# Kernel optimization log

Hardware: AMD Instinct MI355X
Metric: run time of the kernel (lower is better)

Reference implementation:

```python
import jax, jax.numpy as jnp
import numpy as np

B, T, L = 16, 64, 64
DIN, D, DC, A = 512, 512, 512, 256


def setup_inputs() -> dict:
    key = jax.random.key(0)
    ks = jax.random.split(key, 16)
    g = lambda k, shape, fan: jax.random.normal(k, shape, jnp.float32) / np.float32(np.sqrt(fan))
    return {
        "X": jax.random.normal(ks[0], (B, T, DIN), jnp.float32),
        "context": jax.random.normal(ks[1], (B, L, DC), jnp.float32),
        "parent_t_seq": jax.random.randint(ks[2], (B, T), 0, T),
        "context_mask": jnp.zeros((B, L), jnp.int32),
        "mask": jnp.ones((B, T), jnp.float32),
        # fused gate weights, gate order [i, f, c, o] along last axis
        "Wx": g(ks[3], (DIN, 4 * D), DIN),
        "bx": jnp.zeros((4 * D,), jnp.float32),
        "U": g(ks[4], (D, 4 * D), D),
        "C": g(ks[5], (DC, 4 * D), DC),
        "P": g(ks[6], (D, 4 * D), D),
        "H": g(ks[7], (D, 4 * D), D),
        # context attention
        "att_ctx_W1": g(ks[8], (DC, A), DC),
        "att_b1": jnp.zeros((A,), jnp.float32),
        "att_h_W1": g(ks[9], (D, A), D),
        "att_W2": g(ks[10], (A,), A),
        "att_b2": jnp.zeros((), jnp.float32),
        # history attention
        "hatt_hist_W": g(ks[11], (D, A), D),
        "hatt_hist_b": jnp.zeros((A,), jnp.float32),
        "hatt_h_W1": g(ks[12], (D, A), D),
        "hatt_W2": g(ks[13], (A,), A),
        "hatt_b2": jnp.zeros((), jnp.float32),
    }


def reference(X, context, parent_t_seq, context_mask, mask,
              Wx, bx, U, C, P, H,
              att_ctx_W1, att_b1, att_h_W1, att_W2, att_b2,
              hatt_hist_W, hatt_hist_b, hatt_h_W1, hatt_W2, hatt_b2):
    Bb, Tt, _ = X.shape
    Dd = U.shape[0]
    x4 = X @ Wx + bx                                 # [B,T,4D] precomputed input gates
    ctx_trans = context @ att_ctx_W1 + att_b1        # [B,L,A]
    ts = jnp.arange(Tt)
    batch_idx = jnp.arange(Bb)

    def step(carry, inp):
        h, c, hist = carry                           # h,c [B,D]; hist [B,T,D]
        t, xg, m, par = inp                          # xg [B,4D], m [B], par [B]
        # --- attention over encoder context ---
        ah = jnp.tanh(ctx_trans + (h @ att_h_W1)[:, None, :])   # [B,L,A]
        raw = ah @ att_W2 + att_b2                               # [B,L]
        raw = jnp.where(context_mask > 0, -jnp.inf, raw)
        catt = jax.nn.softmax(raw, axis=-1)
        ctx_vec = jnp.einsum('bl,blc->bc', catt, context)        # [B,DC]
        # --- attention over decoding history (positions < t) ---
        hh = jnp.tanh(hist @ hatt_hist_W + hatt_hist_b + (h @ hatt_h_W1)[:, None, :])  # [B,T,A]
        hraw = hh @ hatt_W2 + hatt_b2                            # [B,T]
        hmask = (ts < t).astype(X.dtype)                         # [T]
        hexp = jnp.exp(hraw - jnp.max(hraw, axis=-1, keepdims=True)) * hmask
        hw = hexp / (jnp.sum(hexp, axis=-1, keepdims=True) + 1e-7)
        h_ctx = jnp.where(t > 0, jnp.einsum('bt,btd->bd', hw, hist), 0.0)
        # --- parent hidden state feed ---
        par_h = jnp.where(t > 0, hist[batch_idx, par], 0.0)      # [B,D]
        # --- fused LSTM gates (tree attention path: U, C, P, H terms) ---
        g = xg + h @ U + ctx_vec @ C + par_h @ P + h_ctx @ H     # [B,4D]
        gi, gf, gc, go = jnp.split(g, 4, axis=-1)
        i = jax.nn.sigmoid(gi)
        f = jax.nn.sigmoid(gf)
        o = jax.nn.sigmoid(go)
        c_new = f * c + i * jnp.tanh(gc)
        h_new = o * jnp.tanh(c_new)
        mm = m[:, None]
        h_new = (1 - mm) * h + mm * h_new
        c_new = (1 - mm) * c + mm * c_new
        hist = jax.lax.dynamic_update_slice(hist, h_new[:, None, :], (0, t, 0))
        return (h_new, c_new, hist), (h_new, c_new, ctx_vec)

    h0 = jnp.zeros((Bb, Dd), X.dtype)
    c0 = jnp.zeros((Bb, Dd), X.dtype)
    hist0 = jnp.zeros((Bb, Tt, Dd), X.dtype)
    xs = (ts, jnp.swapaxes(x4, 0, 1), mask.T, parent_t_seq.T)
    _, (hs, cs, ctxs) = jax.lax.scan(step, (h0, c0, hist0), xs)
    # back to batch-major
    return (jnp.swapaxes(hs, 0, 1), jnp.swapaxes(cs, 0, 1), jnp.swapaxes(ctxs, 0, 1))
```

## Files before the change

### kernel.cpp

```cpp
#include <hip/hip_runtime.h>
#include <cmath>

#define NWG 256
#define NT  256

#define WS_FLAGS 0
#define WS_HC    8192
#define WS_CT    16384
#define WS_CACHE 278528
#define WS_HIST  540672

#define OUT_HS  0
#define OUT_CS  524288
#define OUT_CTX 1048576

#define LDS_WT   0
#define LDS_ZS   20544
#define LDS_SCR  28800
#define LDS_GLD  30848
#define LDS_ATT  30976
#define LDS_FLOATS 32448

typedef float vf4 __attribute__((ext_vector_type(4)));
typedef float vf2 __attribute__((ext_vector_type(2)));

struct CAParams {
  const float* X; const float* ctx; const int* parent; const int* cmask; const float* mask;
  const float* Wx; const float* bx; const float* U; const float* C; const float* P; const float* H;
  const float* acW1; const float* ab1; const float* ahW1; const float* aW2; const float* ab2;
  const float* hhW; const float* hhb; const float* hthW1; const float* hW2; const float* hb2;
  float* out; float* ws;
};

__device__ __forceinline__ float tanh_f(float x) {
  x = fminf(15.f, fmaxf(-15.f, x));
  float e = __expf(2.f * x);
  return (e - 1.f) / (e + 1.f);
}
__device__ __forceinline__ float sigm_f(float x) { return 1.f / (1.f + __expf(-x)); }
__device__ __forceinline__ float wsum(float v) {
  #pragma unroll
  for (int m = 32; m; m >>= 1) v += __shfl_xor(v, m, 64);
  return v;
}
__device__ __forceinline__ float wmax(float v) {
  #pragma unroll
  for (int m = 32; m; m >>= 1) v = fmaxf(v, __shfl_xor(v, m, 64));
  return v;
}
__device__ __forceinline__ float hsum32(float v) {
  #pragma unroll
  for (int m = 16; m; m >>= 1) v += __shfl_xor(v, m, 64);
  return v;
}

__device__ __forceinline__ void bst(float* a, float v) {
  asm volatile("global_store_dword %0, %1, off sc0 sc1" :: "v"(a), "v"(v) : "memory");
}
__device__ __forceinline__ void bst4(float* a, vf4 v) {
  asm volatile("global_store_dwordx4 %0, %1, off sc0 sc1" :: "v"(a), "v"(v) : "memory");
}
__device__ __forceinline__ void bld4x4(vf4* r, const float* p0, const float* p1,
                                       const float* p2, const float* p3) {
  asm volatile(
    "global_load_dwordx4 %0, %4, off sc0 sc1\n"
    "global_load_dwordx4 %1, %5, off sc0 sc1\n"
    "global_load_dwordx4 %2, %6, off sc0 sc1\n"
    "global_load_dwordx4 %3, %7, off sc0 sc1\n"
    "s_waitcnt vmcnt(0)"
    : "=&v"(r[0]), "=&v"(r[1]), "=&v"(r[2]), "=&v"(r[3])
    : "v"(p0), "v"(p1), "v"(p2), "v"(p3) : "memory");
}

__global__ void __launch_bounds__(NT, 1) condatt_kernel(CAParams p) {
  extern __shared__ float lds[];
  float* wt   = lds + LDS_WT;
  float* zs   = lds + LDS_ZS;
  float* scr  = lds + LDS_SCR;
  float* gld  = lds + LDS_GLD;
  float* aw   = lds + LDS_ATT;
  float* av2  = lds + LDS_ATT + 256;
  float* abv  = lds + LDS_ATT + 512;
  float* araw = lds + LDS_ATT + 768;
  float* asmx = lds + LDS_ATT + 832;
  float* arawZ= lds + LDS_ATT + 896;
  float* hst  = lds + LDS_ATT + 960;

  const int tid = threadIdx.x;
  const int wg  = blockIdx.x;
  float* wsp = p.ws;
  unsigned* flags = (unsigned*)wsp;
  unsigned nbar = 0;

  const int base = 2 * ((wg & 7) * 32 + (wg >> 3));

  __threadfence_system();

  const int kh = tid >> 4, sub = tid & 15, bg = sub >> 2, cp = sub & 3;
  float acc[4][2] = {{0.f,0.f},{0.f,0.f},{0.f,0.f},{0.f,0.f}};
  float hprev = 0.f, cprev = 0.f;

  auto gsync = [&]() {
    asm volatile("s_waitcnt vmcnt(0)" ::: "memory");
    __syncthreads();
    ++nbar;
    if (tid == 0)
      __hip_atomic_store(&flags[wg * 16], nbar, __ATOMIC_RELAXED, __HIP_MEMORY_SCOPE_SYSTEM);
    while (__hip_atomic_load(&flags[tid * 16], __ATOMIC_RELAXED, __HIP_MEMORY_SCOPE_SYSTEM) < nbar)
      __builtin_amdgcn_s_sleep(1);
    __syncthreads();
  };

  {
    for (int j = 0; j < 4; ++j) {
      int rid = wg * 4 + j;
      __syncthreads();
      for (int i = tid; i < 512; i += NT) scr[i] = p.ctx[rid * 512 + i];
      __syncthreads();
      float a0 = 0.f, a1 = 0.f, a2 = 0.f, a3 = 0.f;
      for (int c = 0; c < 512; c += 4) {
        a0 += scr[c+0] * p.acW1[(c+0) * 256 + tid];
        a1 += scr[c+1] * p.acW1[(c+1) * 256 + tid];
        a2 += scr[c+2] * p.acW1[(c+2) * 256 + tid];
        a3 += scr[c+3] * p.acW1[(c+3) * 256 + tid];
      }
      bst(wsp + WS_CT + rid * 256 + tid, p.ab1[tid] + ((a0 + a1) + (a2 + a3)));
    }
    __syncthreads();
    const float* mats[5] = {p.Wx, p.U, p.P, p.C, p.H};
    for (int q = 0; q < 4; ++q) {
      for (int r = tid; r < 2560; r += NT) {
        int m = r >> 9, rr = r & 511;
        vf2 v = *(const vf2*)(mats[m] + rr * 2048 + base + 512 * q);
        *(vf2*)(wt + q * 5136 + r * 2) = v;
      }
    }
    if (wg < 16)            { av2[tid] = p.aW2[tid]; }
    else if (wg < 32)       { av2[tid] = p.hW2[tid]; abv[tid] = p.hhb[tid]; }
    #pragma unroll
    for (int j = 0; j < 8; ++j) {
      int i4 = tid + j * NT, b = i4 >> 7, k0 = (i4 << 2) & 511;
      vf4 v = *(const vf4*)(p.X + (b * 64 + 0) * 512 + k0);
      *(vf4*)(zs + b * 516 + k0) = v;
    }
    __syncthreads();
  }

  auto gemm = [&](int comp) {
    const float* wp = wt + cp * 5136 + comp * 1024;
    const float* zb = zs + (bg * 4) * 516;
    #pragma unroll 4
    for (int j = 0; j < 32; ++j) {
      int k = kh + (j << 4);
      vf2 w = *(const vf2*)(wp + k * 2);
      float z0 = zb[k], z1 = zb[516 + k], z2 = zb[1032 + k], z3 = zb[1548 + k];
      acc[0][0] += z0 * w.x; acc[0][1] += z0 * w.y;
      acc[1][0] += z1 * w.x; acc[1][1] += z1 * w.y;
      acc[2][0] += z2 * w.x; acc[2][1] += z2 * w.y;
      acc[3][0] += z3 * w.x; acc[3][1] += z3 * w.y;
    }
  };

  gemm(0);
  gsync();

  for (int t = 0; t < 64; ++t) {
    if (wg < 32) {
      const int b = wg & 15;
      if (tid < 128) {
        vf4 v = {0.f, 0.f, 0.f, 0.f};
        if (t > 0) v = *(const vf4*)(wsp + WS_HIST + (b * 64 + (t - 1)) * 512 + tid * 4);
        *(vf4*)(hst + tid * 4) = v;
      }
      __syncthreads();
      if (wg < 16) {
        float s = 0.f;
        #pragma unroll 8
        for (int k = 0; k < 512; ++k) s += hst[k] * p.ahW1[k * 256 + tid];
        aw[tid] = s;
        __syncthreads();
        {
          int w = tid >> 6, s32 = tid & 31, hi = (tid >> 5) & 1;
          float b2 = *p.ab2;
          for (int l = w * 2 + hi; l < 64; l += 8) {
            float sc = 0.f;
            #pragma unroll
            for (int q = 0; q < 8; ++q) { int a = s32 + (q << 5); sc += av2[a] * tanh_f(wsp[WS_CT + (b * 64 + l) * 256 + a] + aw[a]); }
            sc = hsum32(sc) + b2;
            if (s32 == 0) araw[l] = (p.cmask[b * 64 + l] > 0) ? -INFINITY : sc;
          }
        }
        __syncthreads();
        if (tid < 64) {
          float r = araw[tid];
          float mx = wmax(r);
          float e = __expf(r - mx);
          float sm = wsum(e);
          asmx[tid] = e / sm;
        }
        __syncthreads();
        {
          int db = tid & 127, half = tid >> 7;
          vf4 a0 = {0.f, 0.f, 0.f, 0.f};
          #pragma unroll 4
          for (int l = half; l < 64; l += 2) {
            float ca = asmx[l];
            vf4 cv = *(const vf4*)(p.ctx + (b * 64 + l) * 512 + db * 4);
            a0.x += ca * cv.x; a0.y += ca * cv.y; a0.z += ca * cv.z; a0.w += ca * cv.w;
          }
          *(vf4*)(scr + tid * 4) = a0;
        }
        __syncthreads();
        if (tid < 128) {
          vf4 u = *(vf4*)(scr + tid * 4), v = *(vf4*)(scr + (tid + 128) * 4);
          u.x += v.x; u.y += v.y; u.z += v.z; u.w += v.w;
          bst4(p.out + OUT_CTX + (b * 64 + t) * 512 + tid * 4, u);
        }
      } else {
        float s1 = 0.f, s2 = 0.f;
        #pragma unroll 8
        for (int k = 0; k < 512; ++k) {
          float hv = hst[k];
          s1 += hv * p.hthW1[k * 256 + tid];
          s2 += hv * p.hhW[k * 256 + tid];
        }
        aw[tid] = s1;
        if (t > 0) wsp[WS_CACHE + (b * 64 + (t - 1)) * 256 + tid] = s2;
        __syncthreads();
        {
          int w = tid >> 6, s32 = tid & 31, hi = (tid >> 5) & 1;
          float b2 = *p.hb2;
          for (int l = w * 2 + hi; l < t; l += 8) {
            float sc = 0.f;
            #pragma unroll
            for (int q = 0; q < 8; ++q) { int a = s32 + (q << 5); sc += av2[a] * tanh_f(wsp[WS_CACHE + (b * 64 + l) * 256 + a] + abv[a] + aw[a]); }
            sc = hsum32(sc) + b2;
            if (s32 == 0) araw[l] = sc;
          }
          if (tid < 32) {
            float sc = 0.f;
            #pragma unroll
            for (int q = 0; q < 8; ++q) { int a = tid + (q << 5); sc += av2[a] * tanh_f(abv[a] + aw[a]); }
            sc = hsum32(sc) + b2;
            if (tid == 0) arawZ[0] = sc;
          }
        }
        __syncthreads();
        if (tid < 64) {
          float r = (tid < t) ? araw[tid] : arawZ[0];
          float mx = wmax(r);
          float e = (tid < t) ? __expf(r - mx) : 0.f;
          float sm = wsum(e);
          asmx[tid] = e / (sm + 1e-7f);
        }
        __syncthreads();
        {
          int db = tid & 127, half = tid >> 7;
          vf4 a0 = {0.f, 0.f, 0.f, 0.f};
          #pragma unroll 4
          for (int l = half; l < t; l += 2) {
            float hv = asmx[l];
            vf4 hvv = *(const vf4*)(wsp + WS_HIST + (b * 64 + l) * 512 + db * 4);
            a0.x += hv * hvv.x; a0.y += hv * hvv.y; a0.z += hv * hvv.z; a0.w += hv * hvv.w;
          }
          *(vf4*)(scr + tid * 4) = a0;
        }
        __syncthreads();
        if (tid < 128) {
          vf4 u = *(vf4*)(scr + tid * 4), v = *(vf4*)(scr + (tid + 128) * 4);
          u.x += v.x; u.y += v.y; u.z += v.z; u.w += v.w;
          bst4(wsp + WS_HC + b * 512 + tid * 4, u);
        }
      }
    }
    __syncthreads();
    if (t == 0) {
      vf4 z = {0.f, 0.f, 0.f, 0.f};
      #pragma unroll
      for (int j = 0; j < 8; ++j) {
        int i4 = tid + j * NT, b = i4 >> 7, k0 = (i4 << 2) & 511;
        *(vf4*)(zs + b * 516 + k0) = z;
      }
    } else {
      #pragma unroll
      for (int j = 0; j < 8; ++j) {
        int i4 = tid + j * NT, b = i4 >> 7, k0 = (i4 << 2) & 511;
        vf4 v = *(const vf4*)(wsp + WS_HIST + (b * 64 + (t - 1)) * 512 + k0);
        *(vf4*)(zs + b * 516 + k0) = v;
      }
    }
    __syncthreads();
    gemm(1);
    __syncthreads();
    {
      #pragma unroll
      for (int j = 0; j < 8; ++j) {
        int i4 = tid + j * NT, b = i4 >> 7, k0 = (i4 << 2) & 511;
        int par = p.parent[b * 64 + t];
        vf4 v = {0.f, 0.f, 0.f, 0.f};
        if (t > 0 && par < t) v = *(const vf4*)(wsp + WS_HIST + (b * 64 + par) * 512 + k0);
        *(vf4*)(zs + b * 516 + k0) = v;
      }
    }
    __syncthreads();
    gemm(2);
    gsync();

    {
      #pragma unroll
      for (int j = 0; j < 8; ++j) {
        int i4 = tid + j * NT, b = i4 >> 7, k0 = (i4 << 2) & 511;
        vf4 v = *(const vf4*)(p.out + OUT_CTX + (b * 64 + t) * 512 + k0);
        *(vf4*)(zs + b * 516 + k0) = v;
      }
    }
    __syncthreads();
    gemm(3);
    __syncthreads();
    {
      vf4 r[4];
      #pragma unroll
      for (int h2 = 0; h2 < 2; ++h2) {
        int i0 = tid + (h2*4+0)*NT, i1 = tid + (h2*4+1)*NT, i2 = tid + (h2*4+2)*NT, i3 = tid + (h2*4+3)*NT;
        bld4x4(r,
               wsp + WS_HC + (i0 >> 7) * 512 + ((i0 << 2) & 511),
               wsp + WS_HC + (i1 >> 7) * 512 + ((i1 << 2) & 511),
               wsp + WS_HC + (i2 >> 7) * 512 + ((i2 << 2) & 511),
               wsp + WS_HC + (i3 >> 7) * 512 + ((i3 << 2) & 511));
        *(vf4*)(zs + (i0 >> 7) * 516 + ((i0 << 2) & 511)) = r[0];
        *(vf4*)(zs + (i1 >> 7) * 516 + ((i1 << 2) & 511)) = r[1];
        *(vf4*)(zs + (i2 >> 7) * 516 + ((i2 << 2) & 511)) = r[2];
        *(vf4*)(zs + (i3 >> 7) * 516 + ((i3 << 2) & 511)) = r[3];
      }
    }
    __syncthreads();
    gemm(4);
    {
      float* s8 = scr + (kh * 16 + sub) * 8;
      #pragma unroll
      for (int i = 0; i < 4; ++i) { s8[i*2] = acc[i][0]; s8[i*2+1] = acc[i][1]; acc[i][0] = 0.f; acc[i][1] = 0.f; }
    }
    __syncthreads();
    if (t < 63) {
      #pragma unroll
      for (int j = 0; j < 8; ++j) {
        int i4 = tid + j * NT, b = i4 >> 7, k0 = (i4 << 2) & 511;
        vf4 v = *(const vf4*)(p.X + (b * 64 + (t + 1)) * 512 + k0);
        *(vf4*)(zs + b * 516 + k0) = v;
      }
    }
    if (tid < 128) {
      int b = tid >> 3, c = tid & 7;
      int n = base + (c & 1) + 512 * (c >> 1);
      float g = p.bx[n];
      int sidx = (b >> 2) * 4 + (c >> 1);
      int aidx = (b & 3) * 2 + (c & 1);
      #pragma unroll
      for (int k2 = 0; k2 < 16; ++k2) g += scr[(k2 * 16 + sidx) * 8 + aidx];
      gld[b * 8 + c] = g;
    }
    __syncthreads();
    if (tid < 32) {
      int b = tid >> 1, dj = tid & 1;
      int d = base + dj;
      float gi = gld[b*8 + 0 + dj];
      float gf = gld[b*8 + 2 + dj];
      float gg = gld[b*8 + 4 + dj];
      float go = gld[b*8 + 6 + dj];
      float i_ = sigm_f(gi), f_ = sigm_f(gf), o_ = sigm_f(go);
      float cn = f_ * cprev + i_ * tanh_f(gg);
      float hn = o_ * tanh_f(cn);
      float m_ = p.mask[b * 64 + t];
      hn = (1.f - m_) * hprev + m_ * hn;
      cn = (1.f - m_) * cprev + m_ * cn;
      hprev = hn; cprev = cn;
      bst(wsp + WS_HIST + (b * 64 + t) * 512 + d, hn);
      p.out[OUT_HS + (b * 64 + t) * 512 + d] = hn;
      p.out[OUT_CS + (b * 64 + t) * 512 + d] = cn;
    }
    if (t < 63) {
      gemm(0);
      gsync();
    }
  }
}

extern "C" void kernel_launch(void* const* d_in, const int* in_sizes, int n_in,
                              void* d_out, int out_size, void* d_ws, size_t ws_size,
                              hipStream_t stream) {
  CAParams p;
  p.X      = (const float*)d_in[0];
  p.ctx    = (const float*)d_in[1];
  p.parent = (const int*)  d_in[2];
  p.cmask  = (const int*)  d_in[3];
  p.mask   = (const float*)d_in[4];
  p.Wx = (const float*)d_in[5];  p.bx = (const float*)d_in[6];
  p.U  = (const float*)d_in[7];  p.C  = (const float*)d_in[8];
  p.P  = (const float*)d_in[9];  p.H  = (const float*)d_in[10];
  p.acW1 = (const float*)d_in[11]; p.ab1 = (const float*)d_in[12];
  p.ahW1 = (const float*)d_in[13]; p.aW2 = (const float*)d_in[14]; p.ab2 = (const float*)d_in[15];
  p.hhW  = (const float*)d_in[16]; p.hhb = (const float*)d_in[17];
  p.hthW1= (const float*)d_in[18]; p.hW2 = (const float*)d_in[19]; p.hb2 = (const float*)d_in[20];
  p.out = (float*)d_out;
  p.ws  = (float*)d_ws;

  (void)hipMemsetAsync(d_ws, 0, 16384, stream);

  static_assert(LDS_FLOATS * 4 <= 160 * 1024, "LDS budget");
  (void)hipFuncSetAttribute((const void*)condatt_kernel,
                      hipFuncAttributeMaxDynamicSharedMemorySize, LDS_FLOATS * 4);
  hipLaunchKernelGGL(condatt_kernel, dim3(NWG), dim3(NT), LDS_FLOATS * 4, stream, p);
}
```

Before: 2.266 ms.

## Distribute attention h-projections across all workgroups and overlap with U/P gemms

The per-step projections of h through ahW1, hthW1 and hhW were computed serially by the 32 attention workgroups, each doing a 512x256 matvec. Now every workgroup holds one column of each projection matrix in LDS and computes its slice for all batches. Results are published to workspace and signalled with a separate flag. The attention workgroups wait on that flag only after finishing the U and P gemms, so the projection latency overlaps with gate computation. This adds a second inter-workgroup flag wait and extra global traffic per step.

```diff
diff --git a/kernel.cpp b/kernel.cpp
--- a/kernel.cpp
+++ b/kernel.cpp
@@ -5,10 +5,12 @@
 #define NT  256
 
 #define WS_FLAGS 0
-#define WS_HC    8192
-#define WS_CT    16384
-#define WS_CACHE 278528
-#define WS_HIST  540672
+#define WS_HW1   4096
+#define WS_HW1H  8192
+#define WS_HC    12288
+#define WS_CT    20480
+#define WS_CACHE 282624
+#define WS_HIST  544768
 
 #define OUT_HS  0
 #define OUT_CS  524288
@@ -16,10 +18,11 @@
 
 #define LDS_WT   0
 #define LDS_ZS   20544
-#define LDS_SCR  28800
-#define LDS_GLD  30848
-#define LDS_ATT  30976
-#define LDS_FLOATS 32448
+#define LDS_PC   28800
+#define LDS_SCR  30336
+#define LDS_GLD  32384
+#define LDS_ATT  32512
+#define LDS_FLOATS 33472
 
 typedef float vf4 __attribute__((ext_vector_type(4)));
 typedef float vf2 __attribute__((ext_vector_type(2)));
@@ -59,6 +62,12 @@
 }
 __device__ __forceinline__ void bst4(float* a, vf4 v) {
   asm volatile("global_store_dwordx4 %0, %1, off sc0 sc1" :: "v"(a), "v"(v) : "memory");
+}
+__device__ __forceinline__ vf4 bld4(const float* a) {
+  vf4 v;
+  asm volatile("global_load_dwordx4 %0, %1, off sc0 sc1\n"
+               "s_waitcnt vmcnt(0)" : "=v"(v) : "v"(a) : "memory");
+  return v;
 }
 __device__ __forceinline__ void bld4x4(vf4* r, const float* p0, const float* p1,
                                        const float* p2, const float* p3) {
@@ -76,6 +85,7 @@
   extern __shared__ float lds[];
   float* wt   = lds + LDS_WT;
   float* zs   = lds + LDS_ZS;
+  float* pc   = lds + LDS_PC;
   float* scr  = lds + LDS_SCR;
   float* gld  = lds + LDS_GLD;
   float* aw   = lds + LDS_ATT;
@@ -84,7 +94,6 @@
   float* araw = lds + LDS_ATT + 768;
   float* asmx = lds + LDS_ATT + 832;
   float* arawZ= lds + LDS_ATT + 896;
-  float* hst  = lds + LDS_ATT + 960;
 
   const int tid = threadIdx.x;
   const int wg  = blockIdx.x;
@@ -93,6 +102,7 @@
   unsigned nbar = 0;
 
   const int base = 2 * ((wg & 7) * 32 + (wg >> 3));
+  const int pcol = base >> 1;
 
   __threadfence_system();
 
@@ -135,6 +145,11 @@
         *(vf2*)(wt + q * 5136 + r * 2) = v;
       }
     }
+    const float* pm[3] = {p.ahW1, p.hthW1, p.hhW};
+    for (int i = tid; i < 3 * 512; i += NT) {
+      int m = i >> 9, d = i & 511;
+      pc[i] = pm[m][d * 256 + pcol];
+    }
     if (wg < 16)            { av2[tid] = p.aW2[tid]; }
     else if (wg < 32)       { av2[tid] = p.hW2[tid]; abv[tid] = p.hhb[tid]; }
     #pragma unroll
@@ -165,19 +180,64 @@
   gsync();
 
   for (int t = 0; t < 64; ++t) {
+    __syncthreads();
+    if (t == 0) {
+      vf4 z = {0.f, 0.f, 0.f, 0.f};
+      #pragma unroll
+      for (int j = 0; j < 8; ++j) {
+        int i4 = tid + j * NT, b = i4 >> 7, k0 = (i4 << 2) & 511;
+        *(vf4*)(zs + b * 516 + k0) = z;
+      }
+    } else {
+      #pragma unroll
+      for (int j = 0; j < 8; ++j) {
+        int i4 = tid + j * NT, b = i4 >> 7, k0 = (i4 << 2) & 511;
+        vf4 v = *(const vf4*)(wsp + WS_HIST + (b * 64 + (t - 1)) * 512 + k0);
+        *(vf4*)(zs + b * 516 + k0) = v;
+      }
+    }
+    __syncthreads();
+    {
+      int w = tid >> 6, lane = tid & 63;
+      for (int j = w * 12; j < w * 12 + 12; ++j) {
+        int m = j >> 4, b = j & 15;
+        float s = 0.f;
+        #pragma unroll
+        for (int e = 0; e < 8; ++e) { int k = lane + (e << 6); s += zs[b * 516 + k] * pc[m * 512 + k]; }
+        s = wsum(s);
+        if (lane == 0) {
+          if (m == 0)      bst(wsp + WS_HW1  + b * 256 + pcol, s);
+          else if (m == 1) bst(wsp + WS_HW1H + b * 256 + pcol, s);
+          else if (t > 0)  bst(wsp + WS_CACHE + (b * 64 + (t - 1)) * 256 + pcol, s);
+        }
+      }
+    }
+    asm volatile("s_waitcnt vmcnt(0)" ::: "memory");
+    __syncthreads();
+    if (tid == 0)
+      __hip_atomic_store(&flags[wg * 16 + 1], (unsigned)(t + 1), __ATOMIC_RELAXED, __HIP_MEMORY_SCOPE_SYSTEM);
+    gemm(1);
+    __syncthreads();
+    {
+      #pragma unroll
+      for (int j = 0; j < 8; ++j) {
+        int i4 = tid + j * NT, b = i4 >> 7, k0 = (i4 << 2) & 511;
+        int par = p.parent[b * 64 + t];
+        vf4 v = {0.f, 0.f, 0.f, 0.f};
+        if (t > 0 && par < t) v = *(const vf4*)(wsp + WS_HIST + (b * 64 + par) * 512 + k0);
+        *(vf4*)(zs + b * 516 + k0) = v;
+      }
+    }
+    __syncthreads();
+    gemm(2);
+
     if (wg < 32) {
       const int b = wg & 15;
-      if (tid < 128) {
-        vf4 v = {0.f, 0.f, 0.f, 0.f};
-        if (t > 0) v = *(const vf4*)(wsp + WS_HIST + (b * 64 + (t - 1)) * 512 + tid * 4);
-        *(vf4*)(hst + tid * 4) = v;
-      }
+      while (__hip_atomic_load(&flags[tid * 16 + 1], __ATOMIC_RELAXED, __HIP_MEMORY_SCOPE_SYSTEM) < (unsigned)(t + 1))
+        __builtin_amdgcn_s_sleep(1);
       __syncthreads();
       if (wg < 16) {
-        float s = 0.f;
-        #pragma unroll 8
-        for (int k = 0; k < 512; ++k) s += hst[k] * p.ahW1[k * 256 + tid];
-        aw[tid] = s;
+        if (tid < 64) { vf4 v = bld4(wsp + WS_HW1 + b * 256 + tid * 4); *(vf4*)(aw + tid * 4) = v; }
         __syncthreads();
         {
           int w = tid >> 6, s32 = tid & 31, hi = (tid >> 5) & 1;
@@ -217,15 +277,7 @@
           bst4(p.out + OUT_CTX + (b * 64 + t) * 512 + tid * 4, u);
         }
       } else {
-        float s1 = 0.f, s2 = 0.f;
-        #pragma unroll 8
-        for (int k = 0; k < 512; ++k) {
-          float hv = hst[k];
-          s1 += hv * p.hthW1[k * 256 + tid];
-          s2 += hv * p.hhW[k * 256 + tid];
-        }
-        aw[tid] = s1;
-        if (t > 0) wsp[WS_CACHE + (b * 64 + (t - 1)) * 256 + tid] = s2;
+        if (tid < 64) { vf4 v = bld4(wsp + WS_HW1H + b * 256 + tid * 4); *(vf4*)(aw + tid * 4) = v; }
         __syncthreads();
         {
           int w = tid >> 6, s32 = tid & 31, hi = (tid >> 5) & 1;
@@ -273,37 +325,6 @@
         }
       }
     }
-    __syncthreads();
-    if (t == 0) {
-      vf4 z = {0.f, 0.f, 0.f, 0.f};
-      #pragma unroll
-      for (int j = 0; j < 8; ++j) {
-        int i4 = tid + j * NT, b = i4 >> 7, k0 = (i4 << 2) & 511;
-        *(vf4*)(zs + b * 516 + k0) = z;
-      }
-    } else {
-      #pragma unroll
-      for (int j = 0; j < 8; ++j) {
-        int i4 = tid + j * NT, b = i4 >> 7, k0 = (i4 << 2) & 511;
-        vf4 v = *(const vf4*)(wsp + WS_HIST + (b * 64 + (t - 1)) * 512 + k0);
-        *(vf4*)(zs + b * 516 + k0) = v;
-      }
-    }
-    __syncthreads();
-    gemm(1);
-    __syncthreads();
-    {
-      #pragma unroll
-      for (int j = 0; j < 8; ++j) {
-        int i4 = tid + j * NT, b = i4 >> 7, k0 = (i4 << 2) & 511;
-        int par = p.parent[b * 64 + t];
-        vf4 v = {0.f, 0.f, 0.f, 0.f};
-        if (t > 0 && par < t) v = *(const vf4*)(wsp + WS_HIST + (b * 64 + par) * 512 + k0);
-        *(vf4*)(zs + b * 516 + k0) = v;
-      }
-    }
-    __syncthreads();
-    gemm(2);
     gsync();
 
     {
```

Measured after the change: 2.956 ms. 30.4% more time.

## Pack attention projection weights to bf16 and prefetch h_ctx loads across gemm

Applied to the files above, without the earlier changes.

At startup the kernel converts the hatt_h_W1/hatt_hist_W weights into interleaved bf16 pairs and att_h_W1 into bf16 in workspace. The per-step attention projection loops then read half the bytes per weight from global memory. Separately, the h_ctx row loads for gemm(4) are issued before gemm(3) and waited on afterward, so their latency overlaps with compute. bf16 weights reduce precision in the attention scores, and the in-kernel conversion adds setup work.

```diff
diff --git a/kernel.cpp b/kernel.cpp
--- a/kernel.cpp
+++ b/kernel.cpp
@@ -1,5 +1,6 @@
 #include <hip/hip_runtime.h>
 #include <cmath>
+#include <cstdint>
 
 #define NWG 256
 #define NT  256
@@ -9,6 +10,8 @@
 #define WS_CT    16384
 #define WS_CACHE 278528
 #define WS_HIST  540672
+#define WS_HHP   1064960
+#define WS_AHB   1196032
 
 #define OUT_HS  0
 #define OUT_CS  524288
@@ -53,23 +56,39 @@
   for (int m = 16; m; m >>= 1) v += __shfl_xor(v, m, 64);
   return v;
 }
+__device__ __forceinline__ uint32_t f2bf(float f) {
+  uint32_t u = __float_as_uint(f);
+  return (u + 0x7FFFu + ((u >> 16) & 1u)) >> 16;
+}
 
 __device__ __forceinline__ void bst(float* a, float v) {
   asm volatile("global_store_dword %0, %1, off sc0 sc1" :: "v"(a), "v"(v) : "memory");
 }
+__device__ __forceinline__ void bstu(uint32_t* a, uint32_t v) {
+  asm volatile("global_store_dword %0, %1, off sc0 sc1" :: "v"(a), "v"(v) : "memory");
+}
 __device__ __forceinline__ void bst4(float* a, vf4 v) {
   asm volatile("global_store_dwordx4 %0, %1, off sc0 sc1" :: "v"(a), "v"(v) : "memory");
 }
-__device__ __forceinline__ void bld4x4(vf4* r, const float* p0, const float* p1,
-                                       const float* p2, const float* p3) {
+__device__ __forceinline__ void bld8_issue(vf4* r, const float* q0, const float* q1, const float* q2, const float* q3,
+                                           const float* q4, const float* q5, const float* q6, const float* q7) {
   asm volatile(
-    "global_load_dwordx4 %0, %4, off sc0 sc1\n"
-    "global_load_dwordx4 %1, %5, off sc0 sc1\n"
-    "global_load_dwordx4 %2, %6, off sc0 sc1\n"
-    "global_load_dwordx4 %3, %7, off sc0 sc1\n"
-    "s_waitcnt vmcnt(0)"
-    : "=&v"(r[0]), "=&v"(r[1]), "=&v"(r[2]), "=&v"(r[3])
-    : "v"(p0), "v"(p1), "v"(p2), "v"(p3) : "memory");
+    "global_load_dwordx4 %0, %8, off sc0 sc1\n"
+    "global_load_dwordx4 %1, %9, off sc0 sc1\n"
+    "global_load_dwordx4 %2, %10, off sc0 sc1\n"
+    "global_load_dwordx4 %3, %11, off sc0 sc1\n"
+    "global_load_dwordx4 %4, %12, off sc0 sc1\n"
+    "global_load_dwordx4 %5, %13, off sc0 sc1\n"
+    "global_load_dwordx4 %6, %14, off sc0 sc1\n"
+    "global_load_dwordx4 %7, %15, off sc0 sc1"
+    : "=&v"(r[0]),"=&v"(r[1]),"=&v"(r[2]),"=&v"(r[3]),"=&v"(r[4]),"=&v"(r[5]),"=&v"(r[6]),"=&v"(r[7])
+    : "v"(q0),"v"(q1),"v"(q2),"v"(q3),"v"(q4),"v"(q5),"v"(q6),"v"(q7)
+    : "memory");
+}
+__device__ __forceinline__ void bwait8(vf4* r) {
+  asm volatile("s_waitcnt vmcnt(0)"
+    : "+v"(r[0]),"+v"(r[1]),"+v"(r[2]),"+v"(r[3]),"+v"(r[4]),"+v"(r[5]),"+v"(r[6]),"+v"(r[7])
+    :: "memory");
 }
 
 __global__ void __launch_bounds__(NT, 1) condatt_kernel(CAParams p) {
@@ -135,6 +154,20 @@
         *(vf2*)(wt + q * 5136 + r * 2) = v;
       }
     }
+    {
+      uint32_t* hpd = (uint32_t*)(wsp + WS_HHP);
+      for (int i = wg * NT + tid; i < 131072; i += NWG * NT) {
+        uint32_t lo = f2bf(p.hthW1[i]);
+        uint32_t hi = f2bf(p.hhW[i]);
+        bstu(hpd + i, lo | (hi << 16));
+      }
+      uint32_t* ahd = (uint32_t*)(wsp + WS_AHB);
+      for (int j = wg * NT + tid; j < 65536; j += NWG * NT) {
+        uint32_t lo = f2bf(p.ahW1[j * 2]);
+        uint32_t hi = f2bf(p.ahW1[j * 2 + 1]);
+        bstu(ahd + j, lo | (hi << 16));
+      }
+    }
     if (wg < 16)            { av2[tid] = p.aW2[tid]; }
     else if (wg < 32)       { av2[tid] = p.hW2[tid]; abv[tid] = p.hhb[tid]; }
     #pragma unroll
@@ -174,9 +207,11 @@
       }
       __syncthreads();
       if (wg < 16) {
+        const uint16_t* ahb = (const uint16_t*)(wsp + WS_AHB);
         float s = 0.f;
         #pragma unroll 8
-        for (int k = 0; k < 512; ++k) s += hst[k] * p.ahW1[k * 256 + tid];
+        for (int k = 0; k < 512; ++k)
+          s += hst[k] * __uint_as_float((uint32_t)ahb[k * 256 + tid] << 16);
         aw[tid] = s;
         __syncthreads();
         {
@@ -217,12 +252,14 @@
           bst4(p.out + OUT_CTX + (b * 64 + t) * 512 + tid * 4, u);
         }
       } else {
+        const uint32_t* hp = (const uint32_t*)(wsp + WS_HHP);
         float s1 = 0.f, s2 = 0.f;
         #pragma unroll 8
         for (int k = 0; k < 512; ++k) {
+          uint32_t pk = hp[k * 256 + tid];
           float hv = hst[k];
-          s1 += hv * p.hthW1[k * 256 + tid];
-          s2 += hv * p.hhW[k * 256 + tid];
+          s1 += hv * __uint_as_float(pk << 16);
+          s2 += hv * __uint_as_float(pk & 0xFFFF0000u);
         }
         aw[tid] = s1;
         if (t > 0) wsp[WS_CACHE + (b * 64 + (t - 1)) * 256 + tid] = s2;
@@ -315,24 +352,18 @@
       }
     }
     __syncthreads();
+    vf4 rhc[8];
+    {
+      const float* q[8];
+      #pragma unroll
+      for (int j = 0; j < 8; ++j) { int i4 = tid + j * NT; q[j] = wsp + WS_HC + (i4 >> 7) * 512 + ((i4 << 2) & 511); }
+      bld8_issue(rhc, q[0], q[1], q[2], q[3], q[4], q[5], q[6], q[7]);
+    }
     gemm(3);
     __syncthreads();
-    {
-      vf4 r[4];
-      #pragma unroll
-      for (int h2 = 0; h2 < 2; ++h2) {
-        int i0 = tid + (h2*4+0)*NT, i1 = tid + (h2*4+1)*NT, i2 = tid + (h2*4+2)*NT, i3 = tid + (h2*4+3)*NT;
-        bld4x4(r,
-               wsp + WS_HC + (i0 >> 7) * 512 + ((i0 << 2) & 511),
-               wsp + WS_HC + (i1 >> 7) * 512 + ((i1 << 2) & 511),
-               wsp + WS_HC + (i2 >> 7) * 512 + ((i2 << 2) & 511),
-               wsp + WS_HC + (i3 >> 7) * 512 + ((i3 << 2) & 511));
-        *(vf4*)(zs + (i0 >> 7) * 516 + ((i0 << 2) & 511)) = r[0];
-        *(vf4*)(zs + (i1 >> 7) * 516 + ((i1 << 2) & 511)) = r[1];
-        *(vf4*)(zs + (i2 >> 7) * 516 + ((i2 << 2) & 511)) = r[2];
-        *(vf4*)(zs + (i3 >> 7) * 516 + ((i3 << 2) & 511)) = r[3];
-      }
-    }
+    bwait8(rhc);
+    #pragma unroll
+    for (int j = 0; j < 8; ++j) { int i4 = tid + j * NT; *(vf4*)(zs + (i4 >> 7) * 516 + ((i4 << 2) & 511)) = rhc[j]; }
     __syncthreads();
     gemm(4);
     {
```

New measurement: 2.165 ms. 1.05x faster.
